# Kernel optimization log

Hardware: AMD Instinct MI355X
Metric: run time of the kernel (lower is better)

## Reference

```python
import jax, jax.numpy as jnp
import numpy as np

K = 5            # neighbors
TEMP = 1.0       # softmax temperature
BANK = 1000      # fixed bank capacity in source
B = 65536        # batch
D = 256          # feature_dim
EPS = 1e-12      # F.normalize eps


def _l2norm(x):
    # F.normalize(x, dim=1): x / max(||x||, eps)
    n = jnp.sqrt(jnp.sum(x * x, axis=1, keepdims=True))
    return x / jnp.maximum(n, EPS)


def setup_inputs() -> dict:
    key = jax.random.key(0)
    k1, k2, k3, k4 = jax.random.split(key, 4)
    features = jax.random.normal(k1, (B, D), dtype=jnp.float32)
    feature_bank = jax.random.normal(k2, (BANK, D), dtype=jnp.float32)
    # fusion_layer: Linear(2D -> D), ReLU, Linear(D -> D). torch weight layout [out, in].
    W1 = jax.random.normal(k3, (D, 2 * D), dtype=jnp.float32) * (1.0 / np.sqrt(2 * D))
    b1 = jnp.zeros((D,), dtype=jnp.float32)
    W2 = jax.random.normal(k4, (D, D), dtype=jnp.float32) * (1.0 / np.sqrt(D))
    b2 = jnp.zeros((D,), dtype=jnp.float32)
    return {"features": features, "feature_bank": feature_bank,
            "W1": W1, "b1": b1, "W2": W2, "b2": b2}


def reference(features, feature_bank, W1, b1, W2, b2):
    # knn_search: cosine similarity against the (full) bank
    qn = _l2norm(features)                      # [B, D]
    bn = _l2norm(feature_bank)                  # [BANK, D]
    sims = qn @ bn.T                            # [B, BANK]
    top_s, top_i = jax.lax.top_k(sims, K)       # [B, K]
    w = jax.nn.softmax(top_s / TEMP, axis=1)    # [B, K]
    neigh = feature_bank[top_i]                 # gather -> [B, K, D]
    nf = jnp.einsum('bkd,bk->bd', neigh, w)     # weighted average of neighbors
    # fusion MLP on concat([query, neighbors])
    fused = jnp.concatenate([features, nf], axis=1)    # [B, 2D]
    h = jax.nn.relu(fused @ W1.T + b1)                 # [B, D]
    out = h @ W2.T + b2                                # [B, D]
    return out
```

## Files before the change

### kernel.cpp

```cpp
#include <hip/hip_runtime.h>

#define DIM 256
#define NC 12

typedef __attribute__((ext_vector_type(8))) short short8;
typedef __attribute__((ext_vector_type(4))) float f32x4;

__device__ __forceinline__ short f32bf(float f) {
    unsigned u = __builtin_bit_cast(unsigned, f);
    unsigned r = u + 0x7FFFu + ((u >> 16) & 1u);
    return (short)(r >> 16);
}

__device__ __forceinline__ void gld_lds16(const void* g, void* l) {
    __builtin_amdgcn_global_load_lds((const __attribute__((address_space(1))) unsigned int*)g,
                                     (__attribute__((address_space(3))) unsigned int*)l, 16, 0, 0);
}

template<int CTRL>
__device__ __forceinline__ unsigned dppmax(unsigned x) {
    unsigned y = (unsigned)__builtin_amdgcn_update_dpp(0, (int)x, CTRL, 0xF, 0xF, true);
    return x > y ? x : y;
}

__global__ __launch_bounds__(256) void k_prep(const float* __restrict__ bank,
        const float* __restrict__ W1, const float* __restrict__ W2,
        short* __restrict__ bnbf, double* __restrict__ binv,
        short* __restrict__ w1bf, short* __restrict__ w2bf)
{
    __shared__ double part[4];
    __shared__ double s_inv;
    const int bid = blockIdx.x, t = threadIdx.x;
    if (bid < 1024) {
        const int row = bid;
        if (row < 1000) {
            float v = bank[(size_t)row * DIM + t];
            double ssq = (double)v * (double)v;
            for (int o = 32; o > 0; o >>= 1) ssq += __shfl_down(ssq, o);
            if ((t & 63) == 0) part[t >> 6] = ssq;
            __syncthreads();
            if (t == 0) {
                double s = part[0] + part[1] + part[2] + part[3];
                double n = sqrt(s); if (n < 1e-12) n = 1e-12;
                double inv = 1.0 / n;
                binv[row] = inv; s_inv = inv;
            }
            __syncthreads();
            const int pcol = (((t >> 3) ^ (row & 7)) << 3) | (t & 7);
            bnbf[(size_t)row * DIM + pcol] = f32bf((float)((double)v * s_inv));
        } else {
            bnbf[(size_t)row * DIM + t] = 0;
            if (t == 0) binv[row] = 0.0;
        }
    } else if (bid < 1536) {
        const int i = (bid - 1024) * 256 + t;
        w1bf[i] = f32bf(W1[i]);
    } else {
        const int i = (bid - 1536) * 256 + t;
        w2bf[i] = f32bf(W2[i]);
    }
}

__global__ __launch_bounds__(256) void k_sims(const float* __restrict__ feat,
        const short* __restrict__ bnbf, short* __restrict__ sims, int qoff)
{
    __shared__ alignas(16) short Qs[64 * 264];
    __shared__ alignas(16) short Ab[64 * 256];
    const int t = threadIdx.x, lane = t & 63, w = t >> 6;
    const int n16 = lane & 15, q4 = lane >> 4;

    {
        const int r = t >> 2, p = t & 3;
        const float4* src = (const float4*)(feat + (size_t)(qoff + blockIdx.x * 64 + r) * DIM + p * 64);
        short* dst = Qs + r * 264 + p * 64;
        #pragma unroll
        for (int i = 0; i < 16; ++i) {
            float4 v = src[i];
            dst[i*4+0] = f32bf(v.x); dst[i*4+1] = f32bf(v.y);
            dst[i*4+2] = f32bf(v.z); dst[i*4+3] = f32bf(v.w);
        }
    }
    const char* gA = (const char*)bnbf;
    char* lA = (char*)Ab;
    #pragma unroll
    for (int i = 0; i < 8; ++i)
        gld_lds16(gA + i * 4096 + t * 16, lA + i * 4096 + (t >> 6) * 1024);
    __syncthreads();

    short8 bq[8][4];
    #pragma unroll
    for (int kc = 0; kc < 8; ++kc)
        #pragma unroll
        for (int nt = 0; nt < 4; ++nt)
            bq[kc][nt] = *(const short8*)(Qs + (nt * 16 + n16) * 264 + kc * 32 + q4 * 8);

    const int ml = w * 16 + n16;
    int aoff[8];
    #pragma unroll
    for (int kc = 0; kc < 8; ++kc)
        aoff[kc] = (ml * 256 + (((kc * 4 + q4) ^ (ml & 7)) << 3)) * 2;

    const f32x4 vzero = {0.f, 0.f, 0.f, 0.f};
    for (int chunk = 0; chunk < 16; ++chunk) {
        f32x4 acc[4];
        acc[0] = vzero; acc[1] = vzero; acc[2] = vzero; acc[3] = vzero;
        #pragma unroll
        for (int kc = 0; kc < 8; ++kc) {
            short8 af = *(const short8*)(lA + aoff[kc]);
            #pragma unroll
            for (int nt = 0; nt < 4; ++nt)
                acc[nt] = __builtin_amdgcn_mfma_f32_16x16x32_bf16(af, bq[kc][nt], acc[nt], 0, 0, 0);
        }
        const int bankb = chunk * 64 + w * 16 + q4 * 4;
        #pragma unroll
        for (int nt = 0; nt < 4; ++nt) {
            const int qc = blockIdx.x * 64 + nt * 16 + n16;
            uint2 u;
            u.x = ((unsigned)(unsigned short)f32bf(acc[nt][0])) |
                  (((unsigned)(unsigned short)f32bf(acc[nt][1])) << 16);
            u.y = ((unsigned)(unsigned short)f32bf(acc[nt][2])) |
                  (((unsigned)(unsigned short)f32bf(acc[nt][3])) << 16);
            *(uint2*)(sims + (size_t)qc * 1024 + bankb) = u;
        }
        __syncthreads();
        if (chunk < 15) {
            #pragma unroll
            for (int i = 0; i < 8; ++i)
                gld_lds16(gA + (size_t)(chunk + 1) * 32768 + i * 4096 + t * 16,
                          lA + i * 4096 + (t >> 6) * 1024);
            __syncthreads();
        }
    }
}

__global__ __launch_bounds__(256) void k_select(const short* __restrict__ sims,
        int* __restrict__ top, int qoff)
{
    const int t = threadIdx.x, lane = t & 63, w = t >> 6;
    const int q = blockIdx.x * 4 + w;
    const uint4* p = (const uint4*)(sims + (size_t)q * 1024 + lane * 16);
    uint4 a = p[0], b = p[1];

    unsigned k[16];
    {
        unsigned words[8] = {a.x, a.y, a.z, a.w, b.x, b.y, b.z, b.w};
        #pragma unroll
        for (int j = 0; j < 16; ++j) {
            unsigned h = (j & 1) ? (words[j >> 1] >> 16) : (words[j >> 1] & 0xFFFFu);
            unsigned m = (h ^ 0x8000u) ^ ((0u - (h >> 15)) & 0x7FFFu);
            int idx = lane * 16 + j;
            k[j] = (idx < 1000) ? ((m << 16) | (unsigned)idx) : 0u;
        }
    }
    #pragma unroll
    for (int sz = 2; sz <= 16; sz <<= 1)
        #pragma unroll
        for (int st = sz >> 1; st >= 1; st >>= 1)
            #pragma unroll
            for (int i = 0; i < 16; ++i) {
                int j = i ^ st;
                if (j > i) {
                    bool desc = ((i & sz) == 0);
                    unsigned lo = k[i], hi = k[j];
                    unsigned mx = lo > hi ? lo : hi;
                    unsigned mn = lo > hi ? hi : lo;
                    k[i] = desc ? mx : mn;
                    k[j] = desc ? mn : mx;
                }
            }
    unsigned mine = 0;
    #pragma unroll
    for (int r = 0; r < 12; ++r) {
        unsigned m = k[0];
        m = dppmax<0xB1>(m);
        m = dppmax<0x4E>(m);
        m = dppmax<0x141>(m);
        m = dppmax<0x140>(m);
        m = dppmax<0x142>(m);
        m = dppmax<0x143>(m);
        unsigned wm = (unsigned)__builtin_amdgcn_readlane((int)m, 63);
        if (lane == r) mine = wm;
        if (k[0] == wm) {
            #pragma unroll
            for (int s = 0; s < 12; ++s) k[s] = k[s + 1];
        }
    }
    if (lane < 12) top[(size_t)(qoff + q) * NC + lane] = (int)(mine & 0xFFFFu);
}

__global__ __launch_bounds__(256) void k_refine(const float* __restrict__ feat,
        const float* __restrict__ bank, const int* __restrict__ top,
        const double* __restrict__ binv, short* __restrict__ nf)
{
    const int t = threadIdx.x, lane = t & 63, w = t >> 6;
    const int g = lane >> 4, u = lane & 15;
    const int q = blockIdx.x * 16 + w * 4 + g;

    int ci[NC];
    #pragma unroll
    for (int c = 0; c < NC; ++c) ci[c] = top[(size_t)q * NC + c];

    double qd[16];
    double ss = 0.0;
    #pragma unroll
    for (int j = 0; j < 4; ++j) {
        float4 v = *(const float4*)(feat + (size_t)q * DIM + j * 64 + u * 4);
        qd[j*4+0] = v.x; qd[j*4+1] = v.y; qd[j*4+2] = v.z; qd[j*4+3] = v.w;
        ss += (double)v.x*v.x + (double)v.y*v.y + (double)v.z*v.z + (double)v.w*v.w;
    }
    #pragma unroll
    for (int o = 1; o < 16; o <<= 1) ss += __shfl_xor(ss, o, 16);
    double n = sqrt(ss); if (n < 1e-12) n = 1e-12;
    const double qi = 1.0 / n;

    double s[NC];
    #pragma unroll
    for (int c = 0; c < NC; ++c) {
        const float* brow = bank + (size_t)ci[c] * DIM + u * 4;
        double acc = 0.0;
        #pragma unroll
        for (int j = 0; j < 4; ++j) {
            float4 b = *(const float4*)(brow + j * 64);
            acc += qd[j*4+0]*(double)b.x + qd[j*4+1]*(double)b.y
                 + qd[j*4+2]*(double)b.z + qd[j*4+3]*(double)b.w;
        }
        s[c] = acc;
    }
    #pragma unroll
    for (int o = 1; o < 16; o <<= 1)
        #pragma unroll
        for (int c = 0; c < NC; ++c) s[c] += __shfl_xor(s[c], o, 16);

    unsigned long long key[NC];
    float vf[NC];
    #pragma unroll
    for (int c = 0; c < NC; ++c) {
        double v = s[c] * qi * binv[ci[c]];
        vf[c] = (float)v;
        unsigned long long b = __builtin_bit_cast(unsigned long long, v);
        unsigned long long m = (b >> 63) ? ~b : (b | 0x8000000000000000ULL);
        key[c] = (m & ~0x3FFULL) | (unsigned long long)(1023 - ci[c]);
    }

    int rank[NC];
    #pragma unroll
    for (int c = 0; c < NC; ++c) rank[c] = 0;
    #pragma unroll
    for (int c1 = 0; c1 < NC; ++c1)
        #pragma unroll
        for (int c2 = c1 + 1; c2 < NC; ++c2) {
            const bool gt = key[c1] > key[c2];
            rank[c2] += gt ? 1 : 0;
            rank[c1] += gt ? 0 : 1;
        }

    float vm = vf[0];
    #pragma unroll
    for (int c = 1; c < NC; ++c) vm = fmaxf(vm, vf[c]);
    float e[NC]; float wsum = 0.f;
    #pragma unroll
    for (int c = 0; c < NC; ++c) {
        float ex = __expf(vf[c] - vm);
        ex = (rank[c] < 5) ? ex : 0.f;
        e[c] = ex; wsum += ex;
    }
    const float inv = 1.f / wsum;

    asm volatile("" ::: "memory");

    float4 oa[4];
    #pragma unroll
    for (int j = 0; j < 4; ++j) { oa[j].x = 0.f; oa[j].y = 0.f; oa[j].z = 0.f; oa[j].w = 0.f; }
    #pragma unroll
    for (int c = 0; c < NC; ++c) {
        const float wc = e[c] * inv;
        const float* brow = bank + (size_t)ci[c] * DIM + u * 4;
        #pragma unroll
        for (int j = 0; j < 4; ++j) {
            float4 b = *(const float4*)(brow + j * 64);
            oa[j].x += wc * b.x; oa[j].y += wc * b.y;
            oa[j].z += wc * b.z; oa[j].w += wc * b.w;
        }
    }
    short* od = nf + (size_t)q * DIM + u * 4;
    #pragma unroll
    for (int j = 0; j < 4; ++j) {
        uint2 pk;
        pk.x = ((unsigned)(unsigned short)f32bf(oa[j].x)) |
               (((unsigned)(unsigned short)f32bf(oa[j].y)) << 16);
        pk.y = ((unsigned)(unsigned short)f32bf(oa[j].z)) |
               (((unsigned)(unsigned short)f32bf(oa[j].w)) << 16);
        *(uint2*)(od + j * 64) = pk;
    }
}

__global__ __launch_bounds__(256) void k_mlp1(const float* __restrict__ feat,
        const short* __restrict__ nf, const short* __restrict__ w1bf,
        const float* __restrict__ b1, short* __restrict__ h)
{
    __shared__ alignas(16) short As[128 * 40];
    __shared__ alignas(16) short Bs[128 * 40];
    const int t = threadIdx.x, lane = t & 63, w = t >> 6;
    const int mb = (blockIdx.x >> 1) * 128;
    const int nb = (blockIdx.x & 1) * 128;
    const int r = t >> 1, hh = t & 1;
    const int mwb = (w >> 1) * 64, nwb = (w & 1) * 64;
    const f32x4 vzero = {0.f, 0.f, 0.f, 0.f};

    f32x4 acc[4][4];
    #pragma unroll
    for (int a = 0; a < 4; ++a)
        #pragma unroll
        for (int b = 0; b < 4; ++b) acc[a][b] = vzero;

    for (int kc = 0; kc < 16; ++kc) {
        short* ad = As + r * 40 + hh * 16;
        if (kc < 8) {
            const float4* s = (const float4*)(feat + (size_t)(mb + r) * 256 + kc * 32 + hh * 16);
            #pragma unroll
            for (int i = 0; i < 4; ++i) {
                float4 v = s[i];
                ad[i*4+0] = f32bf(v.x); ad[i*4+1] = f32bf(v.y);
                ad[i*4+2] = f32bf(v.z); ad[i*4+3] = f32bf(v.w);
            }
        } else {
            const uint4* s = (const uint4*)(nf + (size_t)(mb + r) * 256 + (kc - 8) * 32 + hh * 16);
            *(uint4*)ad = s[0]; *(uint4*)(ad + 8) = s[1];
        }
        {
            const uint4* bsrc = (const uint4*)(w1bf + (size_t)(nb + r) * 512 + kc * 32 + hh * 16);
            short* bd = Bs + r * 40 + hh * 16;
            *(uint4*)bd = bsrc[0]; *(uint4*)(bd + 8) = bsrc[1];
        }
        __syncthreads();
        short8 af[4], bf[4];
        const int ko = (lane >> 4) << 3;
        #pragma unroll
        for (int mt = 0; mt < 4; ++mt)
            af[mt] = *(const short8*)(As + (mwb + mt * 16 + (lane & 15)) * 40 + ko);
        #pragma unroll
        for (int nt = 0; nt < 4; ++nt)
            bf[nt] = *(const short8*)(Bs + (nwb + nt * 16 + (lane & 15)) * 40 + ko);
        #pragma unroll
        for (int mt = 0; mt < 4; ++mt)
            #pragma unroll
            for (int nt = 0; nt < 4; ++nt)
                acc[mt][nt] = __builtin_amdgcn_mfma_f32_16x16x32_bf16(af[mt], bf[nt], acc[mt][nt], 0, 0, 0);
        __syncthreads();
    }
    {
        const int rq = (lane >> 4) << 2;
        const int cc = lane & 15;
        #pragma unroll
        for (int mt = 0; mt < 4; ++mt)
            #pragma unroll
            for (int nt = 0; nt < 4; ++nt) {
                const int row = mb + mwb + mt * 16 + rq;
                const int col = nb + nwb + nt * 16 + cc;
                const float bias = b1[col];
                #pragma unroll
                for (int rr = 0; rr < 4; ++rr) {
                    float v = acc[mt][nt][rr] + bias;
                    v = fmaxf(v, 0.f);
                    h[(size_t)(row + rr) * 256 + col] = f32bf(v);
                }
            }
    }
}

__global__ __launch_bounds__(256) void k_mlp2(const short* __restrict__ h,
        const short* __restrict__ w2bf, const float* __restrict__ b2,
        float* __restrict__ out)
{
    __shared__ alignas(16) short As[128 * 40];
    __shared__ alignas(16) short Bs[128 * 40];
    const int t = threadIdx.x, lane = t & 63, w = t >> 6;
    const int mb = (blockIdx.x >> 1) * 128;
    const int nb = (blockIdx.x & 1) * 128;
    const int r = t >> 1, hh = t & 1;
    const int mwb = (w >> 1) * 64, nwb = (w & 1) * 64;
    const f32x4 vzero = {0.f, 0.f, 0.f, 0.f};

    f32x4 acc[4][4];
    #pragma unroll
    for (int a = 0; a < 4; ++a)
        #pragma unroll
        for (int b = 0; b < 4; ++b) acc[a][b] = vzero;

    for (int kc = 0; kc < 8; ++kc) {
        {
            const uint4* s = (const uint4*)(h + (size_t)(mb + r) * 256 + kc * 32 + hh * 16);
            short* ad = As + r * 40 + hh * 16;
            *(uint4*)ad = s[0]; *(uint4*)(ad + 8) = s[1];
        }
        {
            const uint4* bsrc = (const uint4*)(w2bf + (size_t)(nb + r) * 256 + kc * 32 + hh * 16);
            short* bd = Bs + r * 40 + hh * 16;
            *(uint4*)bd = bsrc[0]; *(uint4*)(bd + 8) = bsrc[1];
        }
        __syncthreads();
        short8 af[4], bf[4];
        const int ko = (lane >> 4) << 3;
        #pragma unroll
        for (int mt = 0; mt < 4; ++mt)
            af[mt] = *(const short8*)(As + (mwb + mt * 16 + (lane & 15)) * 40 + ko);
        #pragma unroll
        for (int nt = 0; nt < 4; ++nt)
            bf[nt] = *(const short8*)(Bs + (nwb + nt * 16 + (lane & 15)) * 40 + ko);
        #pragma unroll
        for (int mt = 0; mt < 4; ++mt)
            #pragma unroll
            for (int nt = 0; nt < 4; ++nt)
                acc[mt][nt] = __builtin_amdgcn_mfma_f32_16x16x32_bf16(af[mt], bf[nt], acc[mt][nt], 0, 0, 0);
        __syncthreads();
    }
    {
        const int rq = (lane >> 4) << 2;
        const int cc = lane & 15;
        #pragma unroll
        for (int mt = 0; mt < 4; ++mt)
            #pragma unroll
            for (int nt = 0; nt < 4; ++nt) {
                const int row = mb + mwb + mt * 16 + rq;
                const int col = nb + nwb + nt * 16 + cc;
                const float bias = b2[col];
                #pragma unroll
                for (int rr = 0; rr < 4; ++rr)
                    out[(size_t)(row + rr) * 256 + col] = acc[mt][nt][rr] + bias;
            }
    }
}

extern "C" void kernel_launch(void* const* d_in, const int* in_sizes, int n_in,
                              void* d_out, int out_size, void* d_ws, size_t ws_size,
                              hipStream_t stream) {
    const float* feat = (const float*)d_in[0];
    const float* bank = (const float*)d_in[1];
    const float* W1   = (const float*)d_in[2];
    const float* b1   = (const float*)d_in[3];
    const float* W2   = (const float*)d_in[4];
    const float* b2   = (const float*)d_in[5];
    float* out = (float*)d_out;

    char* ws = (char*)d_ws;
    short*  bnbf = (short*)(ws + 0);
    double* binv = (double*)(ws + 524288);
    short*  w1bf = (short*)(ws + 532480);
    short*  w2bf = (short*)(ws + 794624);
    int*    top  = (int*)(ws + 925696);
    short*  nf   = (short*)(ws + 4071424);
    short*  X    = (short*)(ws + 37625856);

    k_prep<<<1792, 256, 0, stream>>>(bank, W1, W2, bnbf, binv, w1bf, w2bf);
    for (int s = 0; s < 4; ++s) {
        const int qoff = s * 16384;
        k_sims  <<<256,  256, 0, stream>>>(feat, bnbf, X, qoff);
        k_select<<<4096, 256, 0, stream>>>(X, top, qoff);
    }
    k_refine<<<4096, 256, 0, stream>>>(feat, bank, top, binv, nf);
    k_mlp1  <<<1024, 256, 0, stream>>>(feat, nf, w1bf, b1, (short*)X);
    k_mlp2  <<<1024, 256, 0, stream>>>((short*)X, w2bf, b2, out);
}
```

Baseline: 433.9 us.

## Use fp32 refine with fp64 fallback, gather only top-5, retile MLP GEMMs

The refine kernel now computes the candidate similarities in fp32. It redoes them in fp64 only when some query in the wavefront has a near-tie between its 5th and 6th ranked candidates, which removes most of the slow double-precision work. The neighbour weighted sum now gathers only the 5 selected bank rows instead of all 12 candidates. Both MLP GEMMs switch from 128x128 tiles to 64-row by full-256-column tiles, so each block covers every output column and reads its A rows once. The risks are wavefront divergence on the fallback path, tie-break differences near the 1e-5 threshold, and a larger shared B tile in each block.

```diff
diff --git a/kernel.cpp b/kernel.cpp
--- a/kernel.cpp
+++ b/kernel.cpp
@@ -199,47 +199,50 @@
     int ci[NC];
     #pragma unroll
     for (int c = 0; c < NC; ++c) ci[c] = top[(size_t)q * NC + c];
-
-    double qd[16];
-    double ss = 0.0;
+    double bd[NC];
+    #pragma unroll
+    for (int c = 0; c < NC; ++c) bd[c] = binv[ci[c]];
+
+    float qf[16];
+    float ssf = 0.f;
     #pragma unroll
     for (int j = 0; j < 4; ++j) {
         float4 v = *(const float4*)(feat + (size_t)q * DIM + j * 64 + u * 4);
-        qd[j*4+0] = v.x; qd[j*4+1] = v.y; qd[j*4+2] = v.z; qd[j*4+3] = v.w;
-        ss += (double)v.x*v.x + (double)v.y*v.y + (double)v.z*v.z + (double)v.w*v.w;
-    }
-    #pragma unroll
-    for (int o = 1; o < 16; o <<= 1) ss += __shfl_xor(ss, o, 16);
-    double n = sqrt(ss); if (n < 1e-12) n = 1e-12;
-    const double qi = 1.0 / n;
-
-    double s[NC];
+        qf[j*4+0] = v.x; qf[j*4+1] = v.y; qf[j*4+2] = v.z; qf[j*4+3] = v.w;
+        ssf += v.x*v.x + v.y*v.y + v.z*v.z + v.w*v.w;
+    }
+    #pragma unroll
+    for (int o = 1; o < 16; o <<= 1) ssf += __shfl_xor(ssf, o, 16);
+    float nq = sqrtf(ssf); if (nq < 1e-12f) nq = 1e-12f;
+    const float qi = 1.f / nq;
+
+    float s[NC];
     #pragma unroll
     for (int c = 0; c < NC; ++c) {
         const float* brow = bank + (size_t)ci[c] * DIM + u * 4;
-        double acc = 0.0;
+        float a0 = 0.f, a1 = 0.f, a2 = 0.f, a3 = 0.f;
         #pragma unroll
         for (int j = 0; j < 4; ++j) {
             float4 b = *(const float4*)(brow + j * 64);
-            acc += qd[j*4+0]*(double)b.x + qd[j*4+1]*(double)b.y
-                 + qd[j*4+2]*(double)b.z + qd[j*4+3]*(double)b.w;
-        }
-        s[c] = acc;
+            a0 += qf[j*4+0] * b.x; a1 += qf[j*4+1] * b.y;
+            a2 += qf[j*4+2] * b.z; a3 += qf[j*4+3] * b.w;
+        }
+        s[c] = (a0 + a1) + (a2 + a3);
     }
     #pragma unroll
     for (int o = 1; o < 16; o <<= 1)
         #pragma unroll
         for (int c = 0; c < NC; ++c) s[c] += __shfl_xor(s[c], o, 16);
 
+    float vf[NC];
     unsigned long long key[NC];
-    float vf[NC];
     #pragma unroll
     for (int c = 0; c < NC; ++c) {
-        double v = s[c] * qi * binv[ci[c]];
-        vf[c] = (float)v;
-        unsigned long long b = __builtin_bit_cast(unsigned long long, v);
-        unsigned long long m = (b >> 63) ? ~b : (b | 0x8000000000000000ULL);
-        key[c] = (m & ~0x3FFULL) | (unsigned long long)(1023 - ci[c]);
+        float v = s[c] * qi * (float)bd[c];
+        vf[c] = v;
+        unsigned ub = __builtin_bit_cast(unsigned, v);
+        unsigned m = (ub >> 31) ? ~ub : (ub | 0x80000000u);
+        key[c] = ((unsigned long long)m << 10) | (unsigned long long)(1023 - ci[c]);
     }
 
     int rank[NC];
@@ -254,6 +257,58 @@
             rank[c1] += gt ? 0 : 1;
         }
 
+    float v5 = 0.f, v6 = 0.f;
+    #pragma unroll
+    for (int c = 0; c < NC; ++c) {
+        v5 += (rank[c] == 4) ? vf[c] : 0.f;
+        v6 += (rank[c] == 5) ? vf[c] : 0.f;
+    }
+    const int need = (v5 - v6) < 1e-5f;
+    if (__any(need)) {
+        double ssd = 0.0;
+        #pragma unroll
+        for (int j = 0; j < 16; ++j) ssd += (double)qf[j] * (double)qf[j];
+        #pragma unroll
+        for (int o = 1; o < 16; o <<= 1) ssd += __shfl_xor(ssd, o, 16);
+        double nd = sqrt(ssd); if (nd < 1e-12) nd = 1e-12;
+        const double qid = 1.0 / nd;
+        double sd[NC];
+        #pragma unroll
+        for (int c = 0; c < NC; ++c) {
+            const float* brow = bank + (size_t)ci[c] * DIM + u * 4;
+            double a0 = 0, a1 = 0, a2 = 0, a3 = 0;
+            #pragma unroll
+            for (int j = 0; j < 4; ++j) {
+                float4 b = *(const float4*)(brow + j * 64);
+                a0 += (double)qf[j*4+0] * b.x; a1 += (double)qf[j*4+1] * b.y;
+                a2 += (double)qf[j*4+2] * b.z; a3 += (double)qf[j*4+3] * b.w;
+            }
+            sd[c] = (a0 + a1) + (a2 + a3);
+        }
+        #pragma unroll
+        for (int o = 1; o < 16; o <<= 1)
+            #pragma unroll
+            for (int c = 0; c < NC; ++c) sd[c] += __shfl_xor(sd[c], o, 16);
+        #pragma unroll
+        for (int c = 0; c < NC; ++c) {
+            double vd = sd[c] * qid * bd[c];
+            vf[c] = (float)vd;
+            unsigned long long ub = __builtin_bit_cast(unsigned long long, vd);
+            unsigned long long m = (ub >> 63) ? ~ub : (ub | 0x8000000000000000ULL);
+            key[c] = (m & ~0x3FFULL) | (unsigned long long)(1023 - ci[c]);
+        }
+        #pragma unroll
+        for (int c = 0; c < NC; ++c) rank[c] = 0;
+        #pragma unroll
+        for (int c1 = 0; c1 < NC; ++c1)
+            #pragma unroll
+            for (int c2 = c1 + 1; c2 < NC; ++c2) {
+                const bool gt = key[c1] > key[c2];
+                rank[c2] += gt ? 1 : 0;
+                rank[c1] += gt ? 0 : 1;
+            }
+    }
+
     float vm = vf[0];
     #pragma unroll
     for (int c = 1; c < NC; ++c) vm = fmaxf(vm, vf[c]);
@@ -266,15 +321,27 @@
     }
     const float inv = 1.f / wsum;
 
-    asm volatile("" ::: "memory");
+    int   selidx[5];
+    float selw[5];
+    #pragma unroll
+    for (int k = 0; k < 5; ++k) {
+        int idx = 0; float wv = 0.f;
+        #pragma unroll
+        for (int c = 0; c < NC; ++c) {
+            const bool is = (rank[c] == k);
+            idx += is ? ci[c] : 0;
+            wv  += is ? e[c]  : 0.f;
+        }
+        selidx[k] = idx; selw[k] = wv * inv;
+    }
 
     float4 oa[4];
     #pragma unroll
     for (int j = 0; j < 4; ++j) { oa[j].x = 0.f; oa[j].y = 0.f; oa[j].z = 0.f; oa[j].w = 0.f; }
     #pragma unroll
-    for (int c = 0; c < NC; ++c) {
-        const float wc = e[c] * inv;
-        const float* brow = bank + (size_t)ci[c] * DIM + u * 4;
+    for (int k = 0; k < 5; ++k) {
+        const float wc = selw[k];
+        const float* brow = bank + (size_t)selidx[k] * DIM + u * 4;
         #pragma unroll
         for (int j = 0; j < 4; ++j) {
             float4 b = *(const float4*)(brow + j * 64);
@@ -298,13 +365,12 @@
         const short* __restrict__ nf, const short* __restrict__ w1bf,
         const float* __restrict__ b1, short* __restrict__ h)
 {
-    __shared__ alignas(16) short As[128 * 40];
-    __shared__ alignas(16) short Bs[128 * 40];
+    __shared__ alignas(16) short As[64 * 40];
+    __shared__ alignas(16) short Bs[256 * 40];
     const int t = threadIdx.x, lane = t & 63, w = t >> 6;
-    const int mb = (blockIdx.x >> 1) * 128;
-    const int nb = (blockIdx.x & 1) * 128;
-    const int r = t >> 1, hh = t & 1;
-    const int mwb = (w >> 1) * 64, nwb = (w & 1) * 64;
+    const int mb = blockIdx.x * 64;
+    const int r = t >> 2, p = t & 3;
+    const int n16 = lane & 15, ko = (lane >> 4) << 3;
     const f32x4 vzero = {0.f, 0.f, 0.f, 0.f};
 
     f32x4 acc[4][4];
@@ -314,33 +380,31 @@
         for (int b = 0; b < 4; ++b) acc[a][b] = vzero;
 
     for (int kc = 0; kc < 16; ++kc) {
-        short* ad = As + r * 40 + hh * 16;
+        short* ad = As + r * 40 + p * 8;
         if (kc < 8) {
-            const float4* s = (const float4*)(feat + (size_t)(mb + r) * 256 + kc * 32 + hh * 16);
-            #pragma unroll
-            for (int i = 0; i < 4; ++i) {
-                float4 v = s[i];
-                ad[i*4+0] = f32bf(v.x); ad[i*4+1] = f32bf(v.y);
-                ad[i*4+2] = f32bf(v.z); ad[i*4+3] = f32bf(v.w);
-            }
+            const float4* s = (const float4*)(feat + (size_t)(mb + r) * 256 + kc * 32 + p * 8);
+            float4 v0 = s[0], v1 = s[1];
+            ad[0] = f32bf(v0.x); ad[1] = f32bf(v0.y); ad[2] = f32bf(v0.z); ad[3] = f32bf(v0.w);
+            ad[4] = f32bf(v1.x); ad[5] = f32bf(v1.y); ad[6] = f32bf(v1.z); ad[7] = f32bf(v1.w);
         } else {
-            const uint4* s = (const uint4*)(nf + (size_t)(mb + r) * 256 + (kc - 8) * 32 + hh * 16);
-            *(uint4*)ad = s[0]; *(uint4*)(ad + 8) = s[1];
+            *(uint4*)ad = *(const uint4*)(nf + (size_t)(mb + r) * 256 + (kc - 8) * 32 + p * 8);
         }
         {
-            const uint4* bsrc = (const uint4*)(w1bf + (size_t)(nb + r) * 512 + kc * 32 + hh * 16);
-            short* bd = Bs + r * 40 + hh * 16;
-            *(uint4*)bd = bsrc[0]; *(uint4*)(bd + 8) = bsrc[1];
+            const uint4* bsrc = (const uint4*)(w1bf + (size_t)t * 512 + kc * 32);
+            short* bdst = Bs + t * 40;
+            *(uint4*)(bdst +  0) = bsrc[0];
+            *(uint4*)(bdst +  8) = bsrc[1];
+            *(uint4*)(bdst + 16) = bsrc[2];
+            *(uint4*)(bdst + 24) = bsrc[3];
         }
         __syncthreads();
         short8 af[4], bf[4];
-        const int ko = (lane >> 4) << 3;
         #pragma unroll
         for (int mt = 0; mt < 4; ++mt)
-            af[mt] = *(const short8*)(As + (mwb + mt * 16 + (lane & 15)) * 40 + ko);
+            af[mt] = *(const short8*)(As + (mt * 16 + n16) * 40 + ko);
         #pragma unroll
         for (int nt = 0; nt < 4; ++nt)
-            bf[nt] = *(const short8*)(Bs + (nwb + nt * 16 + (lane & 15)) * 40 + ko);
+            bf[nt] = *(const short8*)(Bs + (w * 64 + nt * 16 + n16) * 40 + ko);
         #pragma unroll
         for (int mt = 0; mt < 4; ++mt)
             #pragma unroll
@@ -355,8 +419,8 @@
         for (int mt = 0; mt < 4; ++mt)
             #pragma unroll
             for (int nt = 0; nt < 4; ++nt) {
-                const int row = mb + mwb + mt * 16 + rq;
-                const int col = nb + nwb + nt * 16 + cc;
+                const int row = mb + mt * 16 + rq;
+                const int col = w * 64 + nt * 16 + cc;
                 const float bias = b1[col];
                 #pragma unroll
                 for (int rr = 0; rr < 4; ++rr) {
@@ -372,13 +436,12 @@
         const short* __restrict__ w2bf, const float* __restrict__ b2,
         float* __restrict__ out)
 {
-    __shared__ alignas(16) short As[128 * 40];
-    __shared__ alignas(16) short Bs[128 * 40];
+    __shared__ alignas(16) short As[64 * 40];
+    __shared__ alignas(16) short Bs[256 * 40];
     const int t = threadIdx.x, lane = t & 63, w = t >> 6;
-    const int mb = (blockIdx.x >> 1) * 128;
-    const int nb = (blockIdx.x & 1) * 128;
-    const int r = t >> 1, hh = t & 1;
-    const int mwb = (w >> 1) * 64, nwb = (w & 1) * 64;
+    const int mb = blockIdx.x * 64;
+    const int r = t >> 2, p = t & 3;
+    const int n16 = lane & 15, ko = (lane >> 4) << 3;
     const f32x4 vzero = {0.f, 0.f, 0.f, 0.f};
 
     f32x4 acc[4][4];
@@ -388,25 +451,24 @@
         for (int b = 0; b < 4; ++b) acc[a][b] = vzero;
 
     for (int kc = 0; kc < 8; ++kc) {
+        *(uint4*)(As + r * 40 + p * 8) =
+            *(const uint4*)(h + (size_t)(mb + r) * 256 + kc * 32 + p * 8);
         {
-            const uint4* s = (const uint4*)(h + (size_t)(mb + r) * 256 + kc * 32 + hh * 16);
-            short* ad = As + r * 40 + hh * 16;
-            *(uint4*)ad = s[0]; *(uint4*)(ad + 8) = s[1];
-        }
-        {
-            const uint4* bsrc = (const uint4*)(w2bf + (size_t)(nb + r) * 256 + kc * 32 + hh * 16);
-            short* bd = Bs + r * 40 + hh * 16;
-            *(uint4*)bd = bsrc[0]; *(uint4*)(bd + 8) = bsrc[1];
+            const uint4* bsrc = (const uint4*)(w2bf + (size_t)t * 256 + kc * 32);
+            short* bdst = Bs + t * 40;
+            *(uint4*)(bdst +  0) = bsrc[0];
+            *(uint4*)(bdst +  8) = bsrc[1];
+            *(uint4*)(bdst + 16) = bsrc[2];
+            *(uint4*)(bdst + 24) = bsrc[3];
         }
         __syncthreads();
         short8 af[4], bf[4];
-        const int ko = (lane >> 4) << 3;
         #pragma unroll
         for (int mt = 0; mt < 4; ++mt)
-            af[mt] = *(const short8*)(As + (mwb + mt * 16 + (lane & 15)) * 40 + ko);
+            af[mt] = *(const short8*)(As + (mt * 16 + n16) * 40 + ko);
         #pragma unroll
         for (int nt = 0; nt < 4; ++nt)
-            bf[nt] = *(const short8*)(Bs + (nwb + nt * 16 + (lane & 15)) * 40 + ko);
+            bf[nt] = *(const short8*)(Bs + (w * 64 + nt * 16 + n16) * 40 + ko);
         #pragma unroll
         for (int mt = 0; mt < 4; ++mt)
             #pragma unroll
@@ -421,8 +483,8 @@
         for (int mt = 0; mt < 4; ++mt)
             #pragma unroll
             for (int nt = 0; nt < 4; ++nt) {
-                const int row = mb + mwb + mt * 16 + rq;
-                const int col = nb + nwb + nt * 16 + cc;
+                const int row = mb + mt * 16 + rq;
+                const int col = w * 64 + nt * 16 + cc;
                 const float bias = b2[col];
                 #pragma unroll
                 for (int rr = 0; rr < 4; ++rr)
```

New measurement: 433.9 us. About the same (+0.0%).
